# Kernel optimization log

Measured on AMD Instinct MI355X. Metric: run time of the kernel, lower is better.

Reference implementation:

```python
import jax, jax.numpy as jnp
import numpy as np

E = 16       # num_experts
TOP_K = 2
D = 1024     # emb_dim
H = 1024     # moe_hidden_dim
SH = 2048    # shared_expert_hidden_dim
B, S = 2, 2048
W_SCALE = 0.02  # realistic init scale for weights


def setup_inputs() -> dict:
    key = jax.random.key(0)
    ks = jax.random.split(key, 9)
    return {
        "x": jax.random.normal(ks[0], (B, S, D), jnp.float32),
        "gate_w": jax.random.normal(ks[1], (E, D), jnp.float32) * W_SCALE,
        "w_gate": jax.random.normal(ks[2], (E, H, D), jnp.float32) * W_SCALE,
        "w1": jax.random.normal(ks[3], (E, H, D), jnp.float32) * W_SCALE,
        "w2": jax.random.normal(ks[4], (E, D, H), jnp.float32) * W_SCALE,
        "shared_w_gate": jax.random.normal(ks[5], (SH, D), jnp.float32) * W_SCALE,
        "shared_w1": jax.random.normal(ks[6], (SH, D), jnp.float32) * W_SCALE,
        "shared_w2": jax.random.normal(ks[7], (D, SH), jnp.float32) * W_SCALE,
        "shared_gate_w": jax.random.normal(ks[8], (1, D), jnp.float32) * W_SCALE,
    }


def reference(x, gate_w, w_gate, w1, w2, shared_w_gate, shared_w1, shared_w2, shared_gate_w):
    b, s, d = x.shape
    x2d = x.reshape(-1, d)                       # [N, D]
    n = x2d.shape[0]

    # --- router ---
    logits = x2d @ gate_w.T                      # [N, E]
    probs = jax.nn.softmax(logits, axis=-1)
    topk_p, topk_i = jax.lax.top_k(probs, TOP_K)  # [N, K]
    topk_p = topk_p / jnp.sum(topk_p, axis=-1, keepdims=True)

    # combine weights per (token, expert): zero for non-selected experts
    comb = jnp.zeros((n, E), x2d.dtype).at[jnp.arange(n)[:, None], topk_i].add(topk_p)  # [N, E]

    # --- per-expert gated FFN, accumulated via scan (keeps peak memory at [N,H]) ---
    def step(acc, ws):
        wg, wa, wo, cw = ws                      # [H,D], [H,D], [D,H], [N]
        h = (x2d @ wa.T) * jax.nn.silu(x2d @ wg.T)   # [N, H]
        return acc + cw[:, None] * (h @ wo.T), None

    out, _ = jax.lax.scan(step, jnp.zeros_like(x2d), (w_gate, w1, w2, comb.T))

    # --- shared expert path ---
    sh = (x2d @ shared_w1.T) * jax.nn.silu(x2d @ shared_w_gate.T)  # [N, SH]
    shared_out = sh @ shared_w2.T                                  # [N, D]
    sg = jax.nn.sigmoid(x2d @ shared_gate_w.T)                     # [N, 1]
    out = out + sg * shared_out

    return out.reshape(b, s, d)
```

## Files before the change

kernel.cpp:

```cpp
#include <hip/hip_runtime.h>
#include <stdint.h>

#define E_    16
#define TOPK  2
#define D_    1024
#define H_    1024
#define SH_   2048
#define NTOK  4096
#define BK    32
#define NDESC 80
#define RTOK  16
#define NRBLK (NTOK / RTOK)
#define NSHUP (NTOK/128 * SH_/128)
#define NRTUP (NDESC * H_/128)
#define NSHDN (NTOK/128 * D_/128)
#define NRTDN (NDESC * D_/128)
#define NUPGEMM (NSHUP + NRTUP)
#define NW2F4  (E_*D_*H_/4)
#define NS2F4  (D_*SH_/4)
#define CVT2W2 (NW2F4/4096)
#define CVT2S2 (NS2F4/4096)
#define NCVT2  (CVT2W2 + CVT2S2)

typedef unsigned short u16;
typedef __attribute__((ext_vector_type(8))) __bf16 bf16x8;
typedef __attribute__((ext_vector_type(4))) float  f32x4;

struct CvtTable {
  const float* src[5];
  u16*         dst[5];
  int          start[6];
};

__device__ __forceinline__ u16 f2bf(float f) {
  union { float f; unsigned int u; } v; v.f = f;
  unsigned int u = v.u;
  return (u16)((u + 0x7fffu + ((u >> 16) & 1u)) >> 16);
}

__device__ __forceinline__ void gload16(const void* g, void* l) {
  __builtin_amdgcn_global_load_lds(
      (const __attribute__((address_space(1))) unsigned int*)g,
      (__attribute__((address_space(3))) unsigned int*)l, 16, 0, 0);
}

__device__ __forceinline__ int swz8(int b, int nb) {
  return (b & 7) * (nb >> 3) + (b >> 3);
}

__global__ __launch_bounds__(256) void cvtrouter_k(
    CvtTable ct,
    const float* __restrict__ x, const float* __restrict__ gate_w,
    const float* __restrict__ shared_gate_w,
    int* __restrict__ topk_e, float* __restrict__ topk_w,
    float* __restrict__ sg) {
  __shared__ float xs[RTOK][132];
  __shared__ float lg[RTOK][16];
  __shared__ float sgp[RTOK][16];

  int b   = blockIdx.x;
  int tid = threadIdx.x;

  if (b >= NRBLK) {
    int cb = b - NRBLK;
    int s = 0;
    while (cb >= ct.start[s + 1]) s++;
    int i = (cb - ct.start[s]) * 256 + tid;
    float4 f = ((const float4*)ct.src[s])[i];
    ushort4 o; o.x = f2bf(f.x); o.y = f2bf(f.y); o.z = f2bf(f.z); o.w = f2bf(f.w);
    ((ushort4*)ct.dst[s])[i] = o;
    return;
  }

  int e   = tid >> 4;
  int tt  = tid & 15;
  int t0  = b * RTOK;

  float acc = 0.f, sga = 0.f;
  for (int c = 0; c < D_; c += 128) {
    __syncthreads();
    #pragma unroll
    for (int i = 0; i < 2; i++) {
      int f = i * 256 + tid;
      int r = f >> 5, c4 = f & 31;
      *(float4*)&xs[r][c4 * 4] =
          *(const float4*)&x[(size_t)(t0 + r) * D_ + c + c4 * 4];
    }
    __syncthreads();
    const float* gw = &gate_w[(size_t)e * D_ + c];
    #pragma unroll
    for (int d4 = 0; d4 < 32; d4++) {
      float4 g  = *(const float4*)&gw[d4 * 4];
      float4 xv = *(const float4*)&xs[tt][d4 * 4];
      acc += xv.x * g.x + xv.y * g.y + xv.z * g.z + xv.w * g.w;
    }
    #pragma unroll
    for (int j = 0; j < 8; j += 4) {
      float4 s2 = *(const float4*)&shared_gate_w[c + e * 8 + j];
      float4 xv = *(const float4*)&xs[tt][e * 8 + j];
      sga += xv.x * s2.x + xv.y * s2.y + xv.z * s2.z + xv.w * s2.w;
    }
  }
  lg[tt][e]  = acc;
  sgp[tt][e] = sga;
  __syncthreads();

  if (tid < RTOK) {
    int t = t0 + tid;
    float l[16];
    #pragma unroll
    for (int k = 0; k < 16; k++) l[k] = lg[tid][k];
    int i0 = 0; float l0 = l[0];
    for (int k = 1; k < 16; k++) if (l[k] > l0) { l0 = l[k]; i0 = k; }
    int i1 = -1; float l1 = -3.4e38f;
    for (int k = 0; k < 16; k++) if (k != i0 && l[k] > l1) { l1 = l[k]; i1 = k; }
    float w0 = 1.f / (1.f + expf(l1 - l0));
    float s = 0.f;
    #pragma unroll
    for (int k = 0; k < 16; k++) s += sgp[tid][k];
    topk_e[2*t] = i0; topk_e[2*t+1] = i1;
    topk_w[2*t] = w0; topk_w[2*t+1] = 1.f - w0;
    sg[t] = 1.f / (1.f + expf(-s));
  }
}

__global__ __launch_bounds__(256) void scan_scatter_k(
    const int* __restrict__ topk_e, const float* __restrict__ topk_w,
    int* __restrict__ counts, int* __restrict__ offs,
    int* __restrict__ desc_e, int* __restrict__ desc_m,
    int* __restrict__ tok_of, float* __restrict__ w_of) {
  __shared__ int hc[256][E_];
  __shared__ int etot[E_];
  int tid = threadIdx.x;
  #pragma unroll
  for (int e = 0; e < E_; e++) hc[tid][e] = 0;
  __syncthreads();

  for (int i = 0; i < 16; i++) {
    int t = tid * 16 + i;
    hc[tid][topk_e[2*t]]++;
    hc[tid][topk_e[2*t+1]]++;
  }
  __syncthreads();

  if (tid < E_) {
    int run = 0;
    for (int k = 0; k < 256; k++) { int c = hc[k][tid]; hc[k][tid] = run; run += c; }
    etot[tid] = run;
  }
  __syncthreads();

  if (tid == 0) {
    int s = 0, n = 0;
    for (int e = 0; e < E_; e++) {
      offs[e] = s; counts[e] = etot[e];
      for (int m0 = 0; m0 < etot[e]; m0 += 128) { desc_e[n] = e; desc_m[n] = m0; n++; }
      s += etot[e];
    }
    offs[E_] = s;
    for (; n < NDESC; n++) { desc_e[n] = -1; desc_m[n] = 0; }
  }
  __syncthreads();

  for (int i = 0; i < 16; i++) {
    int t = tid * 16 + i;
    #pragma unroll
    for (int k = 0; k < TOPK; k++) {
      int e = topk_e[2*t+k];
      int p = hc[tid][e]++;
      int slot = offs[e] + p;
      tok_of[slot] = t;
      w_of[slot]   = topk_w[2*t+k];
    }
  }
}

__global__ __launch_bounds__(256, 2) void up_merged(
    const u16* __restrict__ Xb,
    const u16* __restrict__ sWg, const u16* __restrict__ sW1, u16* __restrict__ sHout,
    const u16* __restrict__ rWg_all, const u16* __restrict__ rW1_all, u16* __restrict__ rHout,
    const float* __restrict__ w2f, u16* __restrict__ wb2,
    const float* __restrict__ s2f, u16* __restrict__ sb2,
    const int* __restrict__ tok_of,
    const int* __restrict__ offs, const int* __restrict__ counts,
    const int* __restrict__ desc_e, const int* __restrict__ desc_m) {
  int bid = blockIdx.x;
  if (bid >= NUPGEMM) {
    int cb = bid - NUPGEMM;
    const float4* src; ushort4* dst; int base;
    if (cb < CVT2W2) { src = (const float4*)w2f; dst = (ushort4*)wb2; base = cb * 4096; }
    else             { src = (const float4*)s2f; dst = (ushort4*)sb2; base = (cb - CVT2W2) * 4096; }
    int tid = threadIdx.x;
    #pragma unroll
    for (int i = 0; i < 16; i++) {
      int idx = base + i * 256 + tid;
      float4 f = src[idx];
      ushort4 o; o.x = f2bf(f.x); o.y = f2bf(f.y); o.z = f2bf(f.z); o.w = f2bf(f.w);
      dst[idx] = o;
    }
    return;
  }

  const u16 *Wg, *W1; u16* Hout; int Hdim;
  int m0, cnt, pbase, n0;
  const int* tof;
  if (bid < NSHUP) {
    int l = swz8(bid, NSHUP);
    int bx = l >> 4, by = l & 15;
    m0 = bx * 128; cnt = NTOK; pbase = 0; tof = nullptr;
    Wg = sWg; W1 = sW1; Hout = sHout; Hdim = SH_;
    n0 = by * 128;
  } else {
    int r = bid - NSHUP;
    int l = swz8(r, NRTUP);
    int bx = l >> 3, by = l & 7;
    int e = desc_e[bx];
    if (e < 0) return;
    m0 = desc_m[bx]; cnt = counts[e]; pbase = offs[e]; tof = tok_of;
    Wg = rWg_all + (size_t)e * H_ * D_;
    W1 = rW1_all + (size_t)e * H_ * D_;
    Hout = rHout; Hdim = H_;
    n0 = by * 128;
  }

  __shared__ u16 smem[2 * 3 * 4096];

  int tid  = threadIdx.x;
  int lane = tid & 63, wave = tid >> 6;
  int wm = wave & 1, wn = wave >> 1;
  int l16 = lane & 15, quad = lane >> 4;

  int sr = wave * 16 + (lane >> 2);
  int sc = (lane & 3) * 8;

  int gm0 = m0 + sr;      if (gm0 >= cnt) gm0 = cnt - 1;
  int gm1 = m0 + sr + 64; if (gm1 >= cnt) gm1 = cnt - 1;
  int tok0 = tof ? tof[pbase + gm0] : gm0;
  int tok1 = tof ? tof[pbase + gm1] : gm1;
  const u16* pa0 = Xb + (size_t)tok0 * D_ + sc;
  const u16* pa1 = Xb + (size_t)tok1 * D_ + sc;
  const u16* pg0 = Wg + (size_t)(n0 + sr) * D_ + sc;
  const u16* pg1 = pg0 + (size_t)64 * D_;
  const u16* pu0 = W1 + (size_t)(n0 + sr) * D_ + sc;
  const u16* pu1 = pu0 + (size_t)64 * D_;

  int lbase = wave * 512;

  f32x4 accg[4][4], accu[4][4];
  f32x4 zero = {0.f, 0.f, 0.f, 0.f};
  #pragma unroll
  for (int i = 0; i < 4; i++)
    #pragma unroll
    for (int j = 0; j < 4; j++) { accg[i][j] = zero; accu[i][j] = zero; }

#define STAGE_UP(b) do {                                            \
    u16* s_ = smem + (b) * 12288 + lbase;                           \
    gload16(pa0, s_);        gload16(pa1, s_ + 2048);               \
    gload16(pg0, s_ + 4096); gload16(pg1, s_ + 6144);               \
    gload16(pu0, s_ + 8192); gload16(pu1, s_ + 10240);              \
    pa0 += BK; pa1 += BK; pg0 += BK; pg1 += BK; pu0 += BK; pu1 += BK; \
  } while (0)

  STAGE_UP(0);
  STAGE_UP(1);
  int buf = 0;
  const int nt = D_ / BK;

  for (int t = 0; t < nt; ++t) {
    if (t + 1 < nt) asm volatile("s_waitcnt vmcnt(6)" ::: "memory");
    else            asm volatile("s_waitcnt vmcnt(0)" ::: "memory");
    __builtin_amdgcn_s_barrier();
    __builtin_amdgcn_sched_barrier(0);

    const u16* base = smem + buf * 12288;
    bf16x8 af[4], gf[4], uf[4];
    #pragma unroll
    for (int i = 0; i < 4; i++) {
      af[i] = *(const bf16x8*)&base[(wm*64 + i*16 + l16)*BK + quad*8];
      gf[i] = *(const bf16x8*)&base[4096 + (wn*64 + i*16 + l16)*BK + quad*8];
      uf[i] = *(const bf16x8*)&base[8192 + (wn*64 + i*16 + l16)*BK + quad*8];
    }
    #pragma unroll
    for (int i = 0; i < 4; i++)
      #pragma unroll
      for (int j = 0; j < 4; j++) {
        accg[i][j] = __builtin_amdgcn_mfma_f32_16x16x32_bf16(af[i], gf[j], accg[i][j], 0, 0, 0);
        accu[i][j] = __builtin_amdgcn_mfma_f32_16x16x32_bf16(af[i], uf[j], accu[i][j], 0, 0, 0);
      }

    __builtin_amdgcn_sched_barrier(0);
    __builtin_amdgcn_s_barrier();
    if (t + 2 < nt) STAGE_UP(buf);
    buf ^= 1;
  }
#undef STAGE_UP

  #pragma unroll
  for (int i = 0; i < 4; i++) {
    #pragma unroll
    for (int r = 0; r < 4; r++) {
      int m = m0 + wm*64 + i*16 + quad*4 + r;
      if (m < cnt) {
        size_t prow = (size_t)(pbase + m) * Hdim;
        #pragma unroll
        for (int j = 0; j < 4; j++) {
          int n = n0 + wn*64 + j*16 + l16;
          float g = accg[i][j][r];
          float u = accu[i][j][r];
          Hout[prow + n] = f2bf(u * (g / (1.f + expf(-g))));
        }
      }
    }
  }
}

__global__ __launch_bounds__(256, 3) void down_merged(
    const u16* __restrict__ sHbuf, const u16* __restrict__ sW2, const float* __restrict__ sg,
    const u16* __restrict__ rHbuf, const u16* __restrict__ rW2_all, const float* __restrict__ w_of,
    float* __restrict__ out,
    const int* __restrict__ tok_of,
    const int* __restrict__ offs, const int* __restrict__ counts,
    const int* __restrict__ desc_e, const int* __restrict__ desc_m) {
  int bid = blockIdx.x;
  const u16 *Hbuf, *W2; const float* scale;
  int m0, cnt, pbase, n0, K;
  const int* tof;
  if (bid < NSHDN) {
    int l = swz8(bid, NSHDN);
    int bx = l >> 3, by = l & 7;
    m0 = bx * 128; cnt = NTOK; pbase = 0; tof = nullptr;
    Hbuf = sHbuf; W2 = sW2; scale = sg; K = SH_;
    n0 = by * 128;
  } else {
    int r = bid - NSHDN;
    int l = swz8(r, NRTDN);
    int bx = l >> 3, by = l & 7;
    int e = desc_e[bx];
    if (e < 0) return;
    m0 = desc_m[bx]; cnt = counts[e]; pbase = offs[e]; tof = tok_of;
    Hbuf = rHbuf; W2 = rW2_all + (size_t)e * D_ * H_; scale = w_of; K = H_;
    n0 = by * 128;
  }

  __shared__ u16 smem[2 * 2 * 4096];

  int tid  = threadIdx.x;
  int lane = tid & 63, wave = tid >> 6;
  int wm = wave & 1, wn = wave >> 1;
  int l16 = lane & 15, quad = lane >> 4;

  int sr = wave * 16 + (lane >> 2);
  int sc = (lane & 3) * 8;

  int gm0 = m0 + sr;      if (gm0 >= cnt) gm0 = cnt - 1;
  int gm1 = m0 + sr + 64; if (gm1 >= cnt) gm1 = cnt - 1;
  const u16* pa0 = Hbuf + (size_t)(pbase + gm0) * K + sc;
  const u16* pa1 = Hbuf + (size_t)(pbase + gm1) * K + sc;
  const u16* pb0 = W2 + (size_t)(n0 + sr) * K + sc;
  const u16* pb1 = pb0 + (size_t)64 * K;

  int lbase = wave * 512;

  f32x4 acc[4][4];
  f32x4 zero = {0.f, 0.f, 0.f, 0.f};
  #pragma unroll
  for (int i = 0; i < 4; i++)
    #pragma unroll
    for (int j = 0; j < 4; j++) acc[i][j] = zero;

#define STAGE_DN(b) do {                                \
    u16* s_ = smem + (b) * 8192 + lbase;                \
    gload16(pa0, s_);        gload16(pa1, s_ + 2048);   \
    gload16(pb0, s_ + 4096); gload16(pb1, s_ + 6144);   \
    pa0 += BK; pa1 += BK; pb0 += BK; pb1 += BK;         \
  } while (0)

  STAGE_DN(0);
  STAGE_DN(1);
  int buf = 0;
  const int nt = K / BK;

  for (int t = 0; t < nt; ++t) {
    if (t + 1 < nt) asm volatile("s_waitcnt vmcnt(4)" ::: "memory");
    else            asm volatile("s_waitcnt vmcnt(0)" ::: "memory");
    __builtin_amdgcn_s_barrier();
    __builtin_amdgcn_sched_barrier(0);

    const u16* base = smem + buf * 8192;
    bf16x8 af[4], bfr[4];
    #pragma unroll
    for (int i = 0; i < 4; i++) {
      af[i]  = *(const bf16x8*)&base[(wm*64 + i*16 + l16)*BK + quad*8];
      bfr[i] = *(const bf16x8*)&base[4096 + (wn*64 + i*16 + l16)*BK + quad*8];
    }
    #pragma unroll
    for (int i = 0; i < 4; i++)
      #pragma unroll
      for (int j = 0; j < 4; j++)
        acc[i][j] = __builtin_amdgcn_mfma_f32_16x16x32_bf16(af[i], bfr[j], acc[i][j], 0, 0, 0);

    __builtin_amdgcn_sched_barrier(0);
    __builtin_amdgcn_s_barrier();
    if (t + 2 < nt) STAGE_DN(buf);
    buf ^= 1;
  }
#undef STAGE_DN

  #pragma unroll
  for (int i = 0; i < 4; i++) {
    #pragma unroll
    for (int r = 0; r < 4; r++) {
      int m = m0 + wm*64 + i*16 + quad*4 + r;
      if (m < cnt) {
        int p   = pbase + m;
        int tok = tof ? tof[p] : p;
        float sc2 = scale[p];
        #pragma unroll
        for (int j = 0; j < 4; j++) {
          int n = n0 + wn*64 + j*16 + l16;
          atomicAdd(&out[(size_t)tok * D_ + n], sc2 * acc[i][j][r]);
        }
      }
    }
  }
}

extern "C" void kernel_launch(void* const* d_in, const int* in_sizes, int n_in,
                              void* d_out, int out_size, void* d_ws, size_t ws_size,
                              hipStream_t stream) {
  const float* x      = (const float*)d_in[0];
  const float* gate_w = (const float*)d_in[1];
  const float* w_gate = (const float*)d_in[2];
  const float* w1     = (const float*)d_in[3];
  const float* w2     = (const float*)d_in[4];
  const float* sh_wg  = (const float*)d_in[5];
  const float* sh_w1  = (const float*)d_in[6];
  const float* sh_w2  = (const float*)d_in[7];
  const float* sh_gw  = (const float*)d_in[8];
  float* out = (float*)d_out;

  char* ws = (char*)d_ws;
  size_t off = 0;
  u16* xb    = (u16*)(ws + off); off += (size_t)NTOK * D_ * 2;
  u16* h_exp = (u16*)(ws + off); off += (size_t)NTOK * TOPK * H_ * 2;
  u16* h_sh  = (u16*)(ws + off); off += (size_t)NTOK * SH_ * 2;
  u16* wb_g  = (u16*)(ws + off); off += (size_t)E_ * H_ * D_ * 2;
  u16* wb_1  = (u16*)(ws + off); off += (size_t)E_ * H_ * D_ * 2;
  u16* wb_2  = (u16*)(ws + off); off += (size_t)E_ * D_ * H_ * 2;
  u16* sb_g  = (u16*)(ws + off); off += (size_t)SH_ * D_ * 2;
  u16* sb_1  = (u16*)(ws + off); off += (size_t)SH_ * D_ * 2;
  u16* sb_2  = (u16*)(ws + off); off += (size_t)D_ * SH_ * 2;
  int*   tok_of = (int*)  (ws + off); off += NTOK * TOPK * 4;
  float* w_of   = (float*)(ws + off); off += NTOK * TOPK * 4;
  float* sg     = (float*)(ws + off); off += NTOK * 4;
  int*   topk_e = (int*)  (ws + off); off += NTOK * TOPK * 4;
  float* topk_w = (float*)(ws + off); off += NTOK * TOPK * 4;
  int*   counts = (int*)  (ws + off); off += 64;
  int*   offs   = (int*)  (ws + off); off += 128;
  int*   fill   = (int*)  (ws + off); off += 64;
  int*   desc_e = (int*)  (ws + off); off += NDESC * 4;
  int*   desc_m = (int*)  (ws + off); off += NDESC * 4;

  hipMemsetAsync(out, 0, (size_t)NTOK * D_ * 4, stream);

  CvtTable ct;
  const float* srcs[5] = {x, w_gate, w1, sh_wg, sh_w1};
  u16*         dsts[5] = {xb, wb_g, wb_1, sb_g, sb_1};
  int          nblk[5] = {NTOK*D_/1024, E_*H_*D_/1024, E_*H_*D_/1024,
                          SH_*D_/1024, SH_*D_/1024};
  int s = 0;
  for (int i = 0; i < 5; i++) { ct.src[i] = srcs[i]; ct.dst[i] = dsts[i];
                                ct.start[i] = s; s += nblk[i]; }
  ct.start[5] = s;

  cvtrouter_k<<<dim3(NRBLK + s), 256, 0, stream>>>(
      ct, x, gate_w, sh_gw, topk_e, topk_w, sg);
  scan_scatter_k<<<dim3(1), 256, 0, stream>>>(
      topk_e, topk_w, counts, offs, desc_e, desc_m, tok_of, w_of);

  up_merged<<<dim3(NUPGEMM + NCVT2), 256, 0, stream>>>(
      xb, sb_g, sb_1, h_sh, wb_g, wb_1, h_exp,
      w2, wb_2, sh_w2, sb_2,
      tok_of, offs, counts, desc_e, desc_m);
  down_merged<<<dim3(NSHDN + NRTDN), 256, 0, stream>>>(
      h_sh, sb_2, sg, h_exp, wb_2, w_of, out,
      tok_of, offs, counts, desc_e, desc_m);

  (void)in_sizes; (void)n_in; (void)ws_size; (void)fill;
}
```

Baseline: 423.2 us.

## Triple-buffer GEMM LDS pipeline and coarsen fp32-to-bf16 conversion blocks

New measurement: 447.5 us. +5.7%, slower.

```diff
diff --git a/kernel.cpp b/kernel.cpp
--- a/kernel.cpp
+++ b/kernel.cpp
@@ -65,10 +65,16 @@
     int cb = b - NRBLK;
     int s = 0;
     while (cb >= ct.start[s + 1]) s++;
-    int i = (cb - ct.start[s]) * 256 + tid;
-    float4 f = ((const float4*)ct.src[s])[i];
-    ushort4 o; o.x = f2bf(f.x); o.y = f2bf(f.y); o.z = f2bf(f.z); o.w = f2bf(f.w);
-    ((ushort4*)ct.dst[s])[i] = o;
+    const float4* src = (const float4*)ct.src[s];
+    ushort4*      dst = (ushort4*)ct.dst[s];
+    int base = (cb - ct.start[s]) * 4096;
+    #pragma unroll
+    for (int i = 0; i < 16; i++) {
+      int idx = base + i * 256 + tid;
+      float4 f = src[idx];
+      ushort4 o; o.x = f2bf(f.x); o.y = f2bf(f.y); o.z = f2bf(f.z); o.w = f2bf(f.w);
+      dst[idx] = o;
+    }
     return;
   }
 
@@ -223,7 +229,7 @@
     n0 = by * 128;
   }
 
-  __shared__ u16 smem[2 * 3 * 4096];
+  __shared__ u16 smem[3 * 3 * 4096];
 
   int tid  = threadIdx.x;
   int lane = tid & 63, wave = tid >> 6;
@@ -263,16 +269,23 @@
 
   STAGE_UP(0);
   STAGE_UP(1);
-  int buf = 0;
+  int cur = 0;
   const int nt = D_ / BK;
 
   for (int t = 0; t < nt; ++t) {
-    if (t + 1 < nt) asm volatile("s_waitcnt vmcnt(6)" ::: "memory");
-    else            asm volatile("s_waitcnt vmcnt(0)" ::: "memory");
+    if (t + 2 < nt) {
+      int stg = cur ? cur - 1 : 2;
+      STAGE_UP(stg);
+      asm volatile("s_waitcnt vmcnt(12)" ::: "memory");
+    } else if (t + 1 < nt) {
+      asm volatile("s_waitcnt vmcnt(6)" ::: "memory");
+    } else {
+      asm volatile("s_waitcnt vmcnt(0)" ::: "memory");
+    }
     __builtin_amdgcn_s_barrier();
     __builtin_amdgcn_sched_barrier(0);
 
-    const u16* base = smem + buf * 12288;
+    const u16* base = smem + cur * 12288;
     bf16x8 af[4], gf[4], uf[4];
     #pragma unroll
     for (int i = 0; i < 4; i++) {
@@ -290,8 +303,7 @@
 
     __builtin_amdgcn_sched_barrier(0);
     __builtin_amdgcn_s_barrier();
-    if (t + 2 < nt) STAGE_UP(buf);
-    buf ^= 1;
+    cur = (cur == 2) ? 0 : cur + 1;
   }
 #undef STAGE_UP
 
@@ -342,7 +354,7 @@
     n0 = by * 128;
   }
 
-  __shared__ u16 smem[2 * 2 * 4096];
+  __shared__ u16 smem[3 * 2 * 4096];
 
   int tid  = threadIdx.x;
   int lane = tid & 63, wave = tid >> 6;
@@ -377,16 +389,23 @@
 
   STAGE_DN(0);
   STAGE_DN(1);
-  int buf = 0;
+  int cur = 0;
   const int nt = K / BK;
 
   for (int t = 0; t < nt; ++t) {
-    if (t + 1 < nt) asm volatile("s_waitcnt vmcnt(4)" ::: "memory");
-    else            asm volatile("s_waitcnt vmcnt(0)" ::: "memory");
+    if (t + 2 < nt) {
+      int stg = cur ? cur - 1 : 2;
+      STAGE_DN(stg);
+      asm volatile("s_waitcnt vmcnt(8)" ::: "memory");
+    } else if (t + 1 < nt) {
+      asm volatile("s_waitcnt vmcnt(4)" ::: "memory");
+    } else {
+      asm volatile("s_waitcnt vmcnt(0)" ::: "memory");
+    }
     __builtin_amdgcn_s_barrier();
     __builtin_amdgcn_sched_barrier(0);
 
-    const u16* base = smem + buf * 8192;
+    const u16* base = smem + cur * 8192;
     bf16x8 af[4], bfr[4];
     #pragma unroll
     for (int i = 0; i < 4; i++) {
@@ -401,8 +420,7 @@
 
     __builtin_amdgcn_sched_barrier(0);
     __builtin_amdgcn_s_barrier();
-    if (t + 2 < nt) STAGE_DN(buf);
-    buf ^= 1;
+    cur = (cur == 2) ? 0 : cur + 1;
   }
 #undef STAGE_DN
 
@@ -466,8 +484,8 @@
   CvtTable ct;
   const float* srcs[5] = {x, w_gate, w1, sh_wg, sh_w1};
   u16*         dsts[5] = {xb, wb_g, wb_1, sb_g, sb_1};
-  int          nblk[5] = {NTOK*D_/1024, E_*H_*D_/1024, E_*H_*D_/1024,
-                          SH_*D_/1024, SH_*D_/1024};
+  int          nblk[5] = {NTOK*D_/16384, E_*H_*D_/16384, E_*H_*D_/16384,
+                          SH_*D_/16384, SH_*D_/16384};
   int s = 0;
   for (int i = 0; i < 5; i++) { ct.src[i] = srcs[i]; ct.dst[i] = dsts[i];
                                 ct.start[i] = s; s += nblk[i]; }
```

## Use 512-thread blocks in up GEMM and XOR-swizzle LDS reads

Applied to the files above, without the earlier changes.

New measurement: 431.8 us. 1.02x slower.

```diff
diff --git a/kernel.cpp b/kernel.cpp
--- a/kernel.cpp
+++ b/kernel.cpp
@@ -175,7 +175,7 @@
   }
 }
 
-__global__ __launch_bounds__(256, 2) void up_merged(
+__global__ __launch_bounds__(512, 4) void up_merged(
     const u16* __restrict__ Xb,
     const u16* __restrict__ sWg, const u16* __restrict__ sW1, u16* __restrict__ sHout,
     const u16* __restrict__ rWg_all, const u16* __restrict__ rW1_all, u16* __restrict__ rHout,
@@ -185,15 +185,15 @@
     const int* __restrict__ offs, const int* __restrict__ counts,
     const int* __restrict__ desc_e, const int* __restrict__ desc_m) {
   int bid = blockIdx.x;
+  int tid = threadIdx.x;
   if (bid >= NUPGEMM) {
     int cb = bid - NUPGEMM;
     const float4* src; ushort4* dst; int base;
     if (cb < CVT2W2) { src = (const float4*)w2f; dst = (ushort4*)wb2; base = cb * 4096; }
     else             { src = (const float4*)s2f; dst = (ushort4*)sb2; base = (cb - CVT2W2) * 4096; }
-    int tid = threadIdx.x;
-    #pragma unroll
-    for (int i = 0; i < 16; i++) {
-      int idx = base + i * 256 + tid;
+    #pragma unroll
+    for (int i = 0; i < 8; i++) {
+      int idx = base + i * 512 + tid;
       float4 f = src[idx];
       ushort4 o; o.x = f2bf(f.x); o.y = f2bf(f.y); o.z = f2bf(f.z); o.w = f2bf(f.w);
       dst[idx] = o;
@@ -225,40 +225,35 @@
 
   __shared__ u16 smem[2 * 3 * 4096];
 
-  int tid  = threadIdx.x;
   int lane = tid & 63, wave = tid >> 6;
   int wm = wave & 1, wn = wave >> 1;
   int l16 = lane & 15, quad = lane >> 4;
 
-  int sr = wave * 16 + (lane >> 2);
-  int sc = (lane & 3) * 8;
-
-  int gm0 = m0 + sr;      if (gm0 >= cnt) gm0 = cnt - 1;
-  int gm1 = m0 + sr + 64; if (gm1 >= cnt) gm1 = cnt - 1;
-  int tok0 = tof ? tof[pbase + gm0] : gm0;
-  int tok1 = tof ? tof[pbase + gm1] : gm1;
-  const u16* pa0 = Xb + (size_t)tok0 * D_ + sc;
-  const u16* pa1 = Xb + (size_t)tok1 * D_ + sc;
-  const u16* pg0 = Wg + (size_t)(n0 + sr) * D_ + sc;
-  const u16* pg1 = pg0 + (size_t)64 * D_;
-  const u16* pu0 = W1 + (size_t)(n0 + sr) * D_ + sc;
-  const u16* pu1 = pu0 + (size_t)64 * D_;
+  int sr = tid >> 2;
+  int qs = tid & 3;
+  int sc = ((qs ^ ((sr >> 1) & 3))) * 8;
+
+  int gm = m0 + sr; if (gm >= cnt) gm = cnt - 1;
+  int tok = tof ? tof[pbase + gm] : gm;
+  const u16* pa = Xb + (size_t)tok * D_ + sc;
+  const u16* pg = Wg + (size_t)(n0 + sr) * D_ + sc;
+  const u16* pu = W1 + (size_t)(n0 + sr) * D_ + sc;
 
   int lbase = wave * 512;
 
-  f32x4 accg[4][4], accu[4][4];
+  f32x4 accg[4][2], accu[4][2];
   f32x4 zero = {0.f, 0.f, 0.f, 0.f};
   #pragma unroll
   for (int i = 0; i < 4; i++)
     #pragma unroll
-    for (int j = 0; j < 4; j++) { accg[i][j] = zero; accu[i][j] = zero; }
+    for (int j = 0; j < 2; j++) { accg[i][j] = zero; accu[i][j] = zero; }
+
+  int qx8 = (quad ^ ((l16 >> 1) & 3)) * 8;
 
 #define STAGE_UP(b) do {                                            \
     u16* s_ = smem + (b) * 12288 + lbase;                           \
-    gload16(pa0, s_);        gload16(pa1, s_ + 2048);               \
-    gload16(pg0, s_ + 4096); gload16(pg1, s_ + 6144);               \
-    gload16(pu0, s_ + 8192); gload16(pu1, s_ + 10240);              \
-    pa0 += BK; pa1 += BK; pg0 += BK; pg1 += BK; pu0 += BK; pu1 += BK; \
+    gload16(pa, s_); gload16(pg, s_ + 4096); gload16(pu, s_ + 8192);\
+    pa += BK; pg += BK; pu += BK;                                   \
   } while (0)
 
   STAGE_UP(0);
@@ -267,23 +262,25 @@
   const int nt = D_ / BK;
 
   for (int t = 0; t < nt; ++t) {
-    if (t + 1 < nt) asm volatile("s_waitcnt vmcnt(6)" ::: "memory");
+    if (t + 1 < nt) asm volatile("s_waitcnt vmcnt(3)" ::: "memory");
     else            asm volatile("s_waitcnt vmcnt(0)" ::: "memory");
     __builtin_amdgcn_s_barrier();
     __builtin_amdgcn_sched_barrier(0);
 
     const u16* base = smem + buf * 12288;
-    bf16x8 af[4], gf[4], uf[4];
-    #pragma unroll
-    for (int i = 0; i < 4; i++) {
-      af[i] = *(const bf16x8*)&base[(wm*64 + i*16 + l16)*BK + quad*8];
-      gf[i] = *(const bf16x8*)&base[4096 + (wn*64 + i*16 + l16)*BK + quad*8];
-      uf[i] = *(const bf16x8*)&base[8192 + (wn*64 + i*16 + l16)*BK + quad*8];
+    bf16x8 af[4], gf[2], uf[2];
+    #pragma unroll
+    for (int i = 0; i < 4; i++)
+      af[i] = *(const bf16x8*)&base[(wm*64 + i*16 + l16)*BK + qx8];
+    #pragma unroll
+    for (int j = 0; j < 2; j++) {
+      gf[j] = *(const bf16x8*)&base[4096 + (wn*32 + j*16 + l16)*BK + qx8];
+      uf[j] = *(const bf16x8*)&base[8192 + (wn*32 + j*16 + l16)*BK + qx8];
     }
     #pragma unroll
     for (int i = 0; i < 4; i++)
       #pragma unroll
-      for (int j = 0; j < 4; j++) {
+      for (int j = 0; j < 2; j++) {
         accg[i][j] = __builtin_amdgcn_mfma_f32_16x16x32_bf16(af[i], gf[j], accg[i][j], 0, 0, 0);
         accu[i][j] = __builtin_amdgcn_mfma_f32_16x16x32_bf16(af[i], uf[j], accu[i][j], 0, 0, 0);
       }
@@ -303,8 +300,8 @@
       if (m < cnt) {
         size_t prow = (size_t)(pbase + m) * Hdim;
         #pragma unroll
-        for (int j = 0; j < 4; j++) {
-          int n = n0 + wn*64 + j*16 + l16;
+        for (int j = 0; j < 2; j++) {
+          int n = n0 + wn*32 + j*16 + l16;
           float g = accg[i][j][r];
           float u = accu[i][j][r];
           Hout[prow + n] = f2bf(u * (g / (1.f + expf(-g))));
@@ -349,8 +346,9 @@
   int wm = wave & 1, wn = wave >> 1;
   int l16 = lane & 15, quad = lane >> 4;
 
-  int sr = wave * 16 + (lane >> 2);
-  int sc = (lane & 3) * 8;
+  int sr = tid >> 2;
+  int qs = tid & 3;
+  int sc = ((qs ^ ((sr >> 1) & 3))) * 8;
 
   int gm0 = m0 + sr;      if (gm0 >= cnt) gm0 = cnt - 1;
   int gm1 = m0 + sr + 64; if (gm1 >= cnt) gm1 = cnt - 1;
@@ -368,6 +366,8 @@
     #pragma unroll
     for (int j = 0; j < 4; j++) acc[i][j] = zero;
 
+  int qx8 = (quad ^ ((l16 >> 1) & 3)) * 8;
+
 #define STAGE_DN(b) do {                                \
     u16* s_ = smem + (b) * 8192 + lbase;                \
     gload16(pa0, s_);        gload16(pa1, s_ + 2048);   \
@@ -390,8 +390,8 @@
     bf16x8 af[4], bfr[4];
     #pragma unroll
     for (int i = 0; i < 4; i++) {
-      af[i]  = *(const bf16x8*)&base[(wm*64 + i*16 + l16)*BK + quad*8];
-      bfr[i] = *(const bf16x8*)&base[4096 + (wn*64 + i*16 + l16)*BK + quad*8];
+      af[i]  = *(const bf16x8*)&base[(wm*64 + i*16 + l16)*BK + qx8];
+      bfr[i] = *(const bf16x8*)&base[4096 + (wn*64 + i*16 + l16)*BK + qx8];
     }
     #pragma unroll
     for (int i = 0; i < 4; i++)
@@ -478,7 +478,7 @@
   scan_scatter_k<<<dim3(1), 256, 0, stream>>>(
       topk_e, topk_w, counts, offs, desc_e, desc_m, tok_of, w_of);
 
-  up_merged<<<dim3(NUPGEMM + NCVT2), 256, 0, stream>>>(
+  up_merged<<<dim3(NUPGEMM + NCVT2), 512, 0, stream>>>(
       xb, sb_g, sb_1, h_sh, wb_g, wb_1, h_exp,
       w2, wb_2, sh_w2, sb_2,
       tok_of, offs, counts, desc_e, desc_m);
```
